# Performance work log

Measured on AMD Instinct MI355X. Metric: run time of the kernel, lower is better.

The kernel has to match this reference:

```python
import jax, jax.numpy as jnp
import numpy as np

M, N, IN_DIM, NITER = 32, 32, 1024, 100
ALPHA, SIGMA = 0.3, 16.0  # sigma default = max(m, n) / 2
BATCH = 16384


def setup_inputs() -> dict:
    key = jax.random.key(0)
    k1, k2 = jax.random.split(key)
    x = jax.random.normal(k1, (BATCH, IN_DIM), dtype=jnp.float32)
    weights = jax.random.normal(k2, (IN_DIM, M * N), dtype=jnp.float32)
    ii, jj = jnp.meshgrid(jnp.arange(M), jnp.arange(N), indexing='ij')
    locations = jnp.stack([ii.ravel(), jj.ravel()], axis=1).astype(jnp.int32)  # (m*n, 2), row-major like the generator
    return {"x": x, "weights": weights, "locations": locations, "current_iter": 10}


def reference(x, weights, locations, current_iter):
    # x: (B, in_dim); weights: (in_dim, m*n); locations: (m*n, 2)
    B = x.shape[0]
    # Euclidean distances from each sample to each neuron, via ||a-b||^2 expansion
    x2 = jnp.sum(x * x, axis=1, keepdims=True)            # (B, 1)
    w2 = jnp.sum(weights * weights, axis=0)[None, :]      # (1, m*n)
    d2 = jnp.clip(x2 + w2 - 2.0 * (x @ weights), 0.0, None)
    dists = jnp.sqrt(d2)                                  # (B, m*n)
    loss_per = jnp.min(dists, axis=1)                     # (B,)
    bmu_index = jnp.argmin(dists, axis=1)                 # (B,)
    iter_correction = 1.0 - current_iter / NITER
    lr = ALPHA * iter_correction
    sigma = SIGMA * iter_correction
    loc_f = locations.astype(jnp.float32)                 # (m*n, 2)
    bmu_loc = loc_f[bmu_index]                            # (B, 2)
    # squared grid distance of every neuron to each sample's BMU
    dsq = jnp.sum((loc_f[None, :, :] - bmu_loc[:, None, :]) ** 2, axis=2)  # (B, m*n)
    lr_locations = jnp.exp(-dsq / (sigma * sigma)) * lr   # (B, m*n)
    # delta[i,k] = (1/B) * sum_b lr_locations[b,k] * (x[b,i] - weights[i,k])
    # computed without materializing the (B, in_dim, m*n) broadcast tensor
    pos = jnp.einsum('bk,bi->ik', lr_locations, x)        # (in_dim, m*n)
    neg = weights * jnp.sum(lr_locations, axis=0)[None, :]
    delta = (pos - neg) / B
    new_weights = weights + delta
    loss = jnp.sum(loss_per) / B
    return loss, new_weights
```

## Files before the change

kernel.cpp:

```cpp
#include <hip/hip_runtime.h>

typedef unsigned short u16;
typedef short bf16x8 __attribute__((ext_vector_type(8)));
typedef float f32x4 __attribute__((ext_vector_type(4)));

#define BATCH   16384
#define INDIM   1024
#define KNEUR   1024

__device__ __forceinline__ u16 f2bf(float f) {
  union { float f; unsigned u; } v; v.f = f;
  unsigned r = v.u + 0x7FFFu + ((v.u >> 16) & 1u);
  return (u16)(r >> 16);
}
__device__ __forceinline__ float bf2f(u16 h) {
  union { unsigned u; float f; } v; v.u = ((unsigned)h) << 16; return v.f;
}

#define GLDS(gp, lp) __builtin_amdgcn_global_load_lds( \
  (const __attribute__((address_space(1))) void*)(gp), \
  (__attribute__((address_space(3))) void*)(lp), 16, 0, 0)

#define RAWBAR() __builtin_amdgcn_s_barrier()
#define LGKM0() do { asm volatile("s_waitcnt lgkmcnt(0)" ::: "memory"); \
                     __builtin_amdgcn_sched_barrier(0); } while (0)
#define VMC6() asm volatile("s_waitcnt vmcnt(6)" ::: "memory")
#define VMC0() asm volatile("s_waitcnt vmcnt(0)" ::: "memory")

__global__ __launch_bounds__(256)
void k_prep(const float* __restrict__ x, u16* __restrict__ xb, float* __restrict__ x2,
            const float* __restrict__ w, u16* __restrict__ wt, float* __restrict__ w2,
            const int* __restrict__ loc, const int* __restrict__ itp,
            u16* __restrict__ Tb, float* __restrict__ Tf,
            float* __restrict__ Xf, int* __restrict__ cntcur, float* __restrict__ S) {
  __shared__ float tile[64][65];
  __shared__ float red[4][64];
  int bid = blockIdx.x;
  int t = threadIdx.x;
  if (bid < 4096) {
    int row = bid * 4 + (t >> 6);
    int l = t & 63;
    const float* xr = x + (size_t)row * INDIM;
    u16* xbr = xb + (size_t)row * INDIM;
    float s = 0.f;
    #pragma unroll
    for (int seg = 0; seg < 4; ++seg) {
      float4 v = *(const float4*)(xr + seg * 256 + l * 4);
      ushort4 o; o.x = f2bf(v.x); o.y = f2bf(v.y); o.z = f2bf(v.z); o.w = f2bf(v.w);
      *(ushort4*)(xbr + seg * 256 + l * 4) = o;
      s += v.x * v.x + v.y * v.y + v.z * v.z + v.w * v.w;
    }
    for (int m = 32; m; m >>= 1) s += __shfl_xor(s, m, 64);
    if (l == 0) x2[row] = s;
  } else if (bid < 8192) {
    int id = (bid - 4096) * 256 + t;
    int c = id >> 10, k = id & 1023;
    float corr = 1.f - (float)itp[0] / 100.f;
    float lr = 0.3f * corr;
    float sig = 16.f * corr;
    float inv_s2 = 1.f / (sig * sig);
    int di = loc[2 * c] - loc[2 * k];
    int dj = loc[2 * c + 1] - loc[2 * k + 1];
    float v = lr * __expf(-(float)(di * di + dj * dj) * inv_s2);
    Tf[id] = v;
    Tb[id] = f2bf(v);
    Xf[id] = 0.f;
    if (id < 2048) cntcur[id] = 0;
    if (id < 1024) S[id] = 0.f;
  } else if (bid < 8448) {
    int bb = bid - 8192;
    int bi = bb & 15;
    int bj = bb >> 4;
    int tx = t & 63, ty = t >> 6;
    int i0 = bj * 64, k0 = bi * 64;
    for (int r = ty; r < 64; r += 4)
      tile[r][tx] = w[(size_t)(i0 + r) * KNEUR + k0 + tx];
    __syncthreads();
    for (int r = ty; r < 64; r += 4)
      wt[(size_t)(k0 + r) * INDIM + i0 + tx] = f2bf(tile[tx][r]);
  } else {
    int tx = t & 63, ty = t >> 6;
    int k = (bid - 8448) * 64 + tx;
    float s = 0.f;
    for (int i = ty * 256; i < ty * 256 + 256; ++i) {
      float v = w[(size_t)i * KNEUR + k];
      s += v * v;
    }
    red[ty][tx] = s;
    __syncthreads();
    if (ty == 0) w2[k] = red[0][tx] + red[1][tx] + red[2][tx] + red[3][tx];
  }
}

__global__ __launch_bounds__(512, 2)
void k_gemm1_8p(const u16* __restrict__ A, const u16* __restrict__ Bm,
                const float* __restrict__ x2, const float* __restrict__ w2,
                float* __restrict__ pmin, int* __restrict__ pidx) {
  __shared__ __align__(16) u16 lds[2][2][2][128 * 64];
  __shared__ float s_rv[2][256];
  __shared__ int   s_ri[2][256];

  int bid = blockIdx.x;
  int swz = (bid & 7) * 32 + (bid >> 3);
  int mb = swz >> 2, nb = swz & 3;
  int tid = threadIdx.x;
  int lane = tid & 63;
  int wm = (tid >> 6) >> 1, wn = (tid >> 6) & 1;

  const size_t rowA0 = (size_t)mb * 256;
  const size_t rowB0 = (size_t)nb * 256;

  auto STAGE = [&](int u, int op, int qh) {
    if (u >= 16) return;
    const u16* src = (op == 0) ? (A + (rowA0 + qh * 128) * 1024)
                               : (Bm + (rowB0 + qh * 128) * 1024);
    int k0 = u * 64;
    u16* dst0 = &lds[u & 1][op][qh][0];
    #pragma unroll
    for (int j = 0; j < 2; ++j) {
      int s = j * 512 + tid;
      int r = s >> 3;
      int cs = (s & 7) ^ (r & 7);
      GLDS(src + (size_t)r * 1024 + k0 + cs * 8, dst0 + (size_t)s * 8);
    }
  };
  auto LDA = [&](bf16x8 (&a)[2][2], int db, int qm) {
    #pragma unroll
    for (int mt = 0; mt < 2; ++mt)
      #pragma unroll
      for (int kk = 0; kk < 2; ++kk) {
        int row = wm * 32 + mt * 16 + (lane & 15);
        int ch = (kk * 4 + (lane >> 4)) ^ (row & 7);
        a[mt][kk] = *(const bf16x8*)(&lds[db][0][qm][row * 64 + ch * 8]);
      }
  };
  auto LDB = [&](bf16x8 (&b)[4][2], int db, int qn) {
    #pragma unroll
    for (int nt = 0; nt < 4; ++nt)
      #pragma unroll
      for (int kk = 0; kk < 2; ++kk) {
        int row = wn * 64 + nt * 16 + (lane & 15);
        int ch = (kk * 4 + (lane >> 4)) ^ (row & 7);
        b[nt][kk] = *(const bf16x8*)(&lds[db][1][qn][row * 64 + ch * 8]);
      }
  };

  f32x4 acc[2][2][2][4];
  #pragma unroll
  for (int i = 0; i < 2; ++i)
    #pragma unroll
    for (int j = 0; j < 2; ++j)
      #pragma unroll
      for (int m = 0; m < 2; ++m)
        #pragma unroll
        for (int n = 0; n < 4; ++n) {
          acc[i][j][m][n][0] = 0.f; acc[i][j][m][n][1] = 0.f;
          acc[i][j][m][n][2] = 0.f; acc[i][j][m][n][3] = 0.f;
        }

  bf16x8 a[2][2], b0[4][2], b1[4][2];

  #define PHASE(accq, av, bv) do { \
    __builtin_amdgcn_s_setprio(1); \
    _Pragma("unroll") \
    for (int mt = 0; mt < 2; ++mt) \
      _Pragma("unroll") \
      for (int nt = 0; nt < 4; ++nt) \
        _Pragma("unroll") \
        for (int kk = 0; kk < 2; ++kk) \
          accq[mt][nt] = __builtin_amdgcn_mfma_f32_16x16x32_bf16(av[mt][kk], bv[nt][kk], accq[mt][nt], 0, 0, 0); \
    __builtin_amdgcn_s_setprio(0); \
  } while (0)

  STAGE(0, 0, 0); STAGE(0, 1, 1); STAGE(0, 0, 1); STAGE(0, 1, 0);
  STAGE(1, 0, 0); STAGE(1, 1, 1); STAGE(1, 0, 1);
  VMC6();
  RAWBAR();

  for (int t = 0; t < 16; ++t) {
    int db = t & 1;
    LDA(a, db, 0); LDB(b0, db, 0);
    STAGE(t + 1, 1, 0);
    RAWBAR(); LGKM0();
    PHASE(acc[0][0], a, b0);
    RAWBAR();
    LDB(b1, db, 1);
    STAGE(t + 2, 0, 0);
    RAWBAR(); LGKM0();
    PHASE(acc[0][1], a, b1);
    RAWBAR();
    LDA(a, db, 1);
    STAGE(t + 2, 1, 1);
    RAWBAR(); LGKM0();
    PHASE(acc[1][1], a, b1);
    RAWBAR();
    STAGE(t + 2, 0, 1);
    RAWBAR(); LGKM0();
    PHASE(acc[1][0], a, b0);
    if (t < 14) { VMC6(); } else { VMC0(); }
    RAWBAR();
  }

  int g = lane >> 4, li = lane & 15;
  #pragma unroll
  for (int qm = 0; qm < 2; ++qm)
    #pragma unroll
    for (int mt = 0; mt < 2; ++mt)
      #pragma unroll
      for (int rr = 0; rr < 4; ++rr) {
        int lrow = qm * 128 + wm * 32 + mt * 16 + g * 4 + rr;
        float xv = x2[rowA0 + lrow];
        float v = 1e30f; int vi = 0x7fffffff;
        #pragma unroll
        for (int qn = 0; qn < 2; ++qn)
          #pragma unroll
          for (int nt = 0; nt < 4; ++nt) {
            int col = (int)rowB0 + qn * 128 + wn * 64 + nt * 16 + li;
            float d2 = xv + w2[col] - 2.f * acc[qm][qn][mt][nt][rr];
            if (d2 < v) { v = d2; vi = col; }
          }
        #pragma unroll
        for (int m = 1; m < 16; m <<= 1) {
          float ov = __shfl_xor(v, m, 64);
          int oi = __shfl_xor(vi, m, 64);
          if (ov < v || (ov == v && oi < vi)) { v = ov; vi = oi; }
        }
        if (li == 0) { s_rv[wn][lrow] = v; s_ri[wn][lrow] = vi; }
      }
  __syncthreads();
  if (tid < 256) {
    float v0 = s_rv[0][tid], v1 = s_rv[1][tid];
    int i0 = s_ri[0][tid], i1 = s_ri[1][tid];
    float v = v0; int vi = i0;
    if (v1 < v0 || (v1 == v0 && i1 < i0)) { v = v1; vi = i1; }
    size_t brow = rowA0 + tid;
    pmin[brow * 4 + nb] = v;
    pidx[brow * 4 + nb] = vi;
  }
  #undef PHASE
}

__global__ __launch_bounds__(256, 4)
void k_gemm2(const u16* __restrict__ A, const u16* __restrict__ Bm,
             float* __restrict__ P4) {
  __shared__ __align__(16) u16 ldsA[128 * 64];
  __shared__ __align__(16) u16 ldsB[128 * 64];

  int bid = blockIdx.x;
  int ks = bid & 3;
  int tile = bid >> 2;
  int mb = tile >> 3, nb = tile & 7;
  int ktlo = ks * 4, kthi = ktlo + 4;
  int lane = threadIdx.x & 63;
  int wid = threadIdx.x >> 6;
  int wr = wid >> 1, wc = wid & 1;

  f32x4 acc[4][4];
  #pragma unroll
  for (int i = 0; i < 4; ++i)
    #pragma unroll
    for (int j = 0; j < 4; ++j) { acc[i][j][0] = 0.f; acc[i][j][1] = 0.f; acc[i][j][2] = 0.f; acc[i][j][3] = 0.f; }

  const size_t rowA0 = (size_t)mb * 128;
  const size_t rowB0 = (size_t)nb * 128;

  for (int kt = ktlo; kt < kthi; ++kt) {
    int k0 = kt * 64;
    __syncthreads();
    #pragma unroll
    for (int q = 0; q < 4; ++q) {
      int p = q * 256 + wid * 64 + lane;
      int row = p >> 3;
      int clog = (p & 7) ^ (row & 7);
      GLDS(A + (rowA0 + row) * 1024 + k0 + clog * 8,
           ldsA + (size_t)(q * 256 + wid * 64) * 8);
    }
    #pragma unroll
    for (int q = 0; q < 4; ++q) {
      int p = q * 256 + wid * 64 + lane;
      int row = p >> 3;
      int clog = (p & 7) ^ (row & 7);
      GLDS(Bm + (rowB0 + row) * 1024 + k0 + clog * 8,
           ldsB + (size_t)(q * 256 + wid * 64) * 8);
    }
    __syncthreads();
    #pragma unroll
    for (int kk = 0; kk < 2; ++kk) {
      bf16x8 af[4], bfr[4];
      #pragma unroll
      for (int mt = 0; mt < 4; ++mt) {
        int row = wr * 64 + mt * 16 + (lane & 15);
        int ch = (kk * 4 + (lane >> 4)) ^ (row & 7);
        af[mt] = *(const bf16x8*)(ldsA + row * 64 + ch * 8);
      }
      #pragma unroll
      for (int nt = 0; nt < 4; ++nt) {
        int row = wc * 64 + nt * 16 + (lane & 15);
        int ch = (kk * 4 + (lane >> 4)) ^ (row & 7);
        bfr[nt] = *(const bf16x8*)(ldsB + row * 64 + ch * 8);
      }
      #pragma unroll
      for (int mt = 0; mt < 4; ++mt)
        #pragma unroll
        for (int nt = 0; nt < 4; ++nt)
          acc[mt][nt] = __builtin_amdgcn_mfma_f32_16x16x32_bf16(af[mt], bfr[nt], acc[mt][nt], 0, 0, 0);
    }
  }

  float* base = P4 + ((size_t)ks << 20);
  #pragma unroll
  for (int mt = 0; mt < 4; ++mt)
    #pragma unroll
    for (int nt = 0; nt < 4; ++nt)
      #pragma unroll
      for (int r = 0; r < 4; ++r) {
        int i = (int)rowA0 + wr * 64 + mt * 16 + (lane >> 4) * 4 + r;
        int k = (int)rowB0 + wc * 64 + nt * 16 + (lane & 15);
        base[(size_t)i * KNEUR + k] = acc[mt][nt][r];
      }
}

__global__ void k_bmu_count(const float* __restrict__ pmin, const int* __restrict__ pidx,
                            int* __restrict__ bmu, float* __restrict__ lpart,
                            int* __restrict__ cnt) {
  int b = blockIdx.x * 256 + threadIdx.x;
  float v = 1e30f; int vi = 0;
  #pragma unroll
  for (int j = 0; j < 4; ++j) {
    float pv = pmin[(size_t)b * 4 + j];
    if (pv < v) { v = pv; vi = pidx[(size_t)b * 4 + j]; }
  }
  bmu[b] = vi;
  atomicAdd(&cnt[vi], 1);
  float d = sqrtf(fmaxf(v, 0.f));
  __shared__ float red[256];
  red[threadIdx.x] = d;
  __syncthreads();
  for (int s = 128; s > 0; s >>= 1) {
    if (threadIdx.x < s) red[threadIdx.x] += red[threadIdx.x + s];
    __syncthreads();
  }
  if (threadIdx.x == 0) lpart[blockIdx.x] = red[0];
}

__global__ void k_offsets_loss(const int* __restrict__ cnt, int* __restrict__ cursor,
                               float* __restrict__ cntf,
                               const float* __restrict__ lpart, float* __restrict__ out) {
  __shared__ int sc[256];
  int t = threadIdx.x;
  int4 c4 = *(const int4*)(cnt + 4 * t);
  int tsum = c4.x + c4.y + c4.z + c4.w;
  sc[t] = tsum;
  __syncthreads();
  for (int off = 1; off < 256; off <<= 1) {
    int val = sc[t];
    int add = (t >= off) ? sc[t - off] : 0;
    __syncthreads();
    sc[t] = val + add;
    __syncthreads();
  }
  int excl = sc[t] - tsum;
  cursor[4 * t + 0] = excl;
  cursor[4 * t + 1] = excl + c4.x;
  cursor[4 * t + 2] = excl + c4.x + c4.y;
  cursor[4 * t + 3] = excl + c4.x + c4.y + c4.z;
  cntf[4 * t + 0] = (float)c4.x;
  cntf[4 * t + 1] = (float)c4.y;
  cntf[4 * t + 2] = (float)c4.z;
  cntf[4 * t + 3] = (float)c4.w;
  if (t < 64) {
    float l = lpart[t];
    for (int m = 32; m; m >>= 1) l += __shfl_xor(l, m, 64);
    if (t == 0) out[0] = l * (1.f / (float)BATCH);
  }
}

__global__ void k_place_S(const int* __restrict__ bmu, int* __restrict__ cursor,
                          int* __restrict__ perm,
                          const float* __restrict__ cntf, const float* __restrict__ Tf,
                          float* __restrict__ S) {
  int bid = blockIdx.x;
  int t = threadIdx.x;
  if (bid < 64) {
    int b = bid * 256 + t;
    int c = bmu[b];
    int p = atomicAdd(&cursor[c], 1);
    perm[p] = b;
  } else {
    int chunk = bid - 64;
    int cchunk = chunk >> 2;
    int kb = chunk & 3;
    int k = kb * 256 + t;
    float s = 0.f;
    for (int c = cchunk * 64; c < cchunk * 64 + 64; ++c)
      s += cntf[c] * Tf[(size_t)c * KNEUR + k];
    atomicAdd(&S[k], s);
  }
}

__global__ __launch_bounds__(256)
void k_xsum2(const int* __restrict__ perm, const int* __restrict__ bmu,
             const u16* __restrict__ xb, float* __restrict__ Xf) {
  int t = threadIdx.x;
  int m0 = blockIdx.x * 16;
  int pm[16], cl[16];
  #pragma unroll
  for (int j = 0; j < 16; ++j) pm[j] = perm[m0 + j];
  #pragma unroll
  for (int j = 0; j < 16; ++j) cl[j] = bmu[pm[j]];
  float a0 = 0.f, a1 = 0.f, a2 = 0.f, a3 = 0.f;
  int ccur = cl[0];
  #pragma unroll
  for (int j = 0; j < 16; ++j) {
    if (cl[j] != ccur) {
      float* p = Xf + (size_t)ccur * INDIM + 4 * t;
      atomicAdd(p + 0, a0); atomicAdd(p + 1, a1);
      atomicAdd(p + 2, a2); atomicAdd(p + 3, a3);
      a0 = a1 = a2 = a3 = 0.f;
      ccur = cl[j];
    }
    ushort4 v = *(const ushort4*)(xb + (size_t)pm[j] * INDIM + t * 4);
    a0 += bf2f(v.x); a1 += bf2f(v.y); a2 += bf2f(v.z); a3 += bf2f(v.w);
  }
  float* p = Xf + (size_t)ccur * INDIM + 4 * t;
  atomicAdd(p + 0, a0); atomicAdd(p + 1, a1);
  atomicAdd(p + 2, a2); atomicAdd(p + 3, a3);
}

__global__ void k_trans_base(const float* __restrict__ Xf, u16* __restrict__ xst,
                             const float* __restrict__ w, const float* __restrict__ S,
                             float* __restrict__ outw) {
  int bid = blockIdx.x;
  int t = threadIdx.x;
  if (bid < 256) {
    __shared__ float tile[64][65];
    int bc = bid & 15;
    int bi = bid >> 4;
    int tx = t & 63, ty = t >> 6;
    int c0 = bc * 64, i0 = bi * 64;
    for (int r = ty; r < 64; r += 4)
      tile[r][tx] = Xf[(size_t)(c0 + r) * INDIM + i0 + tx];
    __syncthreads();
    for (int r = ty; r < 64; r += 4)
      xst[(size_t)(i0 + r) * KNEUR + c0 + tx] = f2bf(tile[tx][r]);
  } else {
    const float invB = 1.f / (float)BATCH;
    size_t base = ((size_t)(bid - 256) * 256 + t) * 16;
    int k = (int)(base & 1023);
    #pragma unroll
    for (int seg = 0; seg < 4; ++seg) {
      float4 wv = *(const float4*)(w + base + seg * 4);
      float4 sv = *(const float4*)(S + k + seg * 4);
      outw[base + seg * 4 + 0] = wv.x - wv.x * sv.x * invB;
      outw[base + seg * 4 + 1] = wv.y - wv.y * sv.y * invB;
      outw[base + seg * 4 + 2] = wv.z - wv.z * sv.z * invB;
      outw[base + seg * 4 + 3] = wv.w - wv.w * sv.w * invB;
    }
  }
}

__global__ void k_wupd(const float* __restrict__ P4, float* __restrict__ outw) {
  const float invB = 1.f / (float)BATCH;
  int id4 = blockIdx.x * 256 + threadIdx.x;
  size_t base = (size_t)id4 * 4;
  float4 p0 = *(const float4*)(P4 + base);
  float4 p1 = *(const float4*)(P4 + (1u << 20) + base);
  float4 p2 = *(const float4*)(P4 + (2u << 20) + base);
  float4 p3 = *(const float4*)(P4 + (3u << 20) + base);
  outw[base + 0] += (p0.x + p1.x + p2.x + p3.x) * invB;
  outw[base + 1] += (p0.y + p1.y + p2.y + p3.y) * invB;
  outw[base + 2] += (p0.z + p1.z + p2.z + p3.z) * invB;
  outw[base + 3] += (p0.w + p1.w + p2.w + p3.w) * invB;
}

extern "C" void kernel_launch(void* const* d_in, const int* in_sizes, int n_in,
                              void* d_out, int out_size, void* d_ws, size_t ws_size,
                              hipStream_t stream) {
  const float* x = (const float*)d_in[0];
  const float* w = (const float*)d_in[1];
  const int* loc = (const int*)d_in[2];
  const int* it = (const int*)d_in[3];
  float* out = (float*)d_out;

  char* ws = (char*)d_ws;
  size_t off = 0;
  auto alloc = [&](size_t bytes) -> void* {
    void* p = ws + off;
    off += (bytes + 255) & ~(size_t)255;
    return p;
  };
  u16* xb    = (u16*)  alloc((size_t)BATCH * INDIM * 2);
  u16* wt    = (u16*)  alloc((size_t)KNEUR * INDIM * 2);
  u16* Tb    = (u16*)  alloc((size_t)KNEUR * KNEUR * 2);
  float* Tf  = (float*)alloc((size_t)KNEUR * KNEUR * 4);
  u16* xst   = (u16*)  alloc((size_t)INDIM * KNEUR * 2);
  float* x2  = (float*)alloc((size_t)BATCH * 4);
  float* w2  = (float*)alloc((size_t)KNEUR * 4);
  float* pmin= (float*)alloc((size_t)BATCH * 4 * 4);
  int* pidx  = (int*)  alloc((size_t)BATCH * 4 * 4);
  int* bmu   = (int*)  alloc((size_t)BATCH * 4);
  float* cntf= (float*)alloc((size_t)KNEUR * 4);
  float* S   = (float*)alloc((size_t)KNEUR * 4);
  float* lpart=(float*)alloc(64 * 4);
  float* Xf  = (float*)alloc((size_t)KNEUR * INDIM * 4);
  int* cntcur= (int*)  alloc((size_t)2 * KNEUR * 4);
  int* perm  = (int*)  alloc((size_t)BATCH * 4);
  if (off > ws_size) return;

  int* cnt = cntcur;
  int* cursor = cntcur + KNEUR;
  float* outw = out + 1;
  float* P4 = (float*)xb;

  k_prep<<<8464, 256, 0, stream>>>(x, xb, x2, w, wt, w2, loc, it, Tb, Tf, Xf, cntcur, S);
  k_gemm1_8p<<<256, 512, 0, stream>>>(xb, wt, x2, w2, pmin, pidx);
  k_bmu_count<<<64, 256, 0, stream>>>(pmin, pidx, bmu, lpart, cnt);
  k_offsets_loss<<<1, 256, 0, stream>>>(cnt, cursor, cntf, lpart, out);
  k_place_S<<<128, 256, 0, stream>>>(bmu, cursor, perm, cntf, Tf, S);
  k_xsum2<<<BATCH / 16, 256, 0, stream>>>(perm, bmu, xb, Xf);
  k_trans_base<<<512, 256, 0, stream>>>(Xf, xst, w, S, outw);
  k_gemm2<<<256, 256, 0, stream>>>(xst, Tb, P4);
  k_wupd<<<1024, 256, 0, stream>>>(P4, outw);
}
```

Before: 142.7 us.

## Fuse BMU count and offset scan via last-block ticket, widen xsum chunks

Merges the BMU counting kernel and the single-block prefix-scan/loss kernel into one launch, where the last block to finish (found with an atomic ticket) performs the scan. This removes one kernel launch and its gap. It also doubles the samples per block in the Xf accumulation kernel to cut the number of atomics, and adds a partial lgkmcnt wait in the GEMM1 main loop. The ticket counter gets zeroed in prep, and the fusion relies on a threadfence so the last block sees the other blocks' counts.

```diff
diff --git a/kernel.cpp b/kernel.cpp
--- a/kernel.cpp
+++ b/kernel.cpp
@@ -24,6 +24,7 @@
 #define RAWBAR() __builtin_amdgcn_s_barrier()
 #define LGKM0() do { asm volatile("s_waitcnt lgkmcnt(0)" ::: "memory"); \
                      __builtin_amdgcn_sched_barrier(0); } while (0)
+#define LGKM8() asm volatile("s_waitcnt lgkmcnt(8)" ::: "memory")
 #define VMC6() asm volatile("s_waitcnt vmcnt(6)" ::: "memory")
 #define VMC0() asm volatile("s_waitcnt vmcnt(0)" ::: "memory")
 
@@ -65,7 +66,7 @@
     Tf[id] = v;
     Tb[id] = f2bf(v);
     Xf[id] = 0.f;
-    if (id < 2048) cntcur[id] = 0;
+    if (id < 2304) cntcur[id] = 0;
     if (id < 1024) S[id] = 0.f;
   } else if (bid < 8448) {
     int bb = bid - 8192;
@@ -181,6 +182,7 @@
     int db = t & 1;
     LDA(a, db, 0); LDB(b0, db, 0);
     STAGE(t + 1, 1, 0);
+    LGKM8();
     RAWBAR(); LGKM0();
     PHASE(acc[0][0], a, b0);
     RAWBAR();
@@ -320,10 +322,13 @@
       }
 }
 
-__global__ void k_bmu_count(const float* __restrict__ pmin, const int* __restrict__ pidx,
-                            int* __restrict__ bmu, float* __restrict__ lpart,
-                            int* __restrict__ cnt) {
-  int b = blockIdx.x * 256 + threadIdx.x;
+__global__ void k_bmu_scan(const float* __restrict__ pmin, const int* __restrict__ pidx,
+                           int* __restrict__ bmu, float* __restrict__ lpart,
+                           int* __restrict__ cnt, int* __restrict__ ticket,
+                           int* __restrict__ cursor, float* __restrict__ cntf,
+                           float* __restrict__ out) {
+  int t = threadIdx.x;
+  int b = blockIdx.x * 256 + t;
   float v = 1e30f; int vi = 0;
   #pragma unroll
   for (int j = 0; j < 4; ++j) {
@@ -334,20 +339,21 @@
   atomicAdd(&cnt[vi], 1);
   float d = sqrtf(fmaxf(v, 0.f));
   __shared__ float red[256];
-  red[threadIdx.x] = d;
+  red[t] = d;
   __syncthreads();
   for (int s = 128; s > 0; s >>= 1) {
-    if (threadIdx.x < s) red[threadIdx.x] += red[threadIdx.x + s];
-    __syncthreads();
-  }
-  if (threadIdx.x == 0) lpart[blockIdx.x] = red[0];
-}
-
-__global__ void k_offsets_loss(const int* __restrict__ cnt, int* __restrict__ cursor,
-                               float* __restrict__ cntf,
-                               const float* __restrict__ lpart, float* __restrict__ out) {
+    if (t < s) red[t] += red[t + s];
+    __syncthreads();
+  }
+  if (t == 0) lpart[blockIdx.x] = red[0];
+
+  __threadfence();
+  __shared__ int is_last;
+  if (t == 0) is_last = (atomicAdd(ticket, 1) == 63);
+  __syncthreads();
+  if (!is_last) return;
+
   __shared__ int sc[256];
-  int t = threadIdx.x;
   int4 c4 = *(const int4*)(cnt + 4 * t);
   int tsum = c4.x + c4.y + c4.z + c4.w;
   sc[t] = tsum;
@@ -402,16 +408,16 @@
 void k_xsum2(const int* __restrict__ perm, const int* __restrict__ bmu,
              const u16* __restrict__ xb, float* __restrict__ Xf) {
   int t = threadIdx.x;
-  int m0 = blockIdx.x * 16;
-  int pm[16], cl[16];
-  #pragma unroll
-  for (int j = 0; j < 16; ++j) pm[j] = perm[m0 + j];
-  #pragma unroll
-  for (int j = 0; j < 16; ++j) cl[j] = bmu[pm[j]];
+  int m0 = blockIdx.x * 32;
+  int pm[32], cl[32];
+  #pragma unroll
+  for (int j = 0; j < 32; ++j) pm[j] = perm[m0 + j];
+  #pragma unroll
+  for (int j = 0; j < 32; ++j) cl[j] = bmu[pm[j]];
   float a0 = 0.f, a1 = 0.f, a2 = 0.f, a3 = 0.f;
   int ccur = cl[0];
   #pragma unroll
-  for (int j = 0; j < 16; ++j) {
+  for (int j = 0; j < 32; ++j) {
     if (cl[j] != ccur) {
       float* p = Xf + (size_t)ccur * INDIM + 4 * t;
       atomicAdd(p + 0, a0); atomicAdd(p + 1, a1);
@@ -503,21 +509,21 @@
   float* S   = (float*)alloc((size_t)KNEUR * 4);
   float* lpart=(float*)alloc(64 * 4);
   float* Xf  = (float*)alloc((size_t)KNEUR * INDIM * 4);
-  int* cntcur= (int*)  alloc((size_t)2 * KNEUR * 4);
+  int* cntcur= (int*)  alloc((size_t)2304 * 4);
   int* perm  = (int*)  alloc((size_t)BATCH * 4);
   if (off > ws_size) return;
 
   int* cnt = cntcur;
   int* cursor = cntcur + KNEUR;
+  int* ticket = cntcur + 2 * KNEUR;
   float* outw = out + 1;
   float* P4 = (float*)xb;
 
   k_prep<<<8464, 256, 0, stream>>>(x, xb, x2, w, wt, w2, loc, it, Tb, Tf, Xf, cntcur, S);
   k_gemm1_8p<<<256, 512, 0, stream>>>(xb, wt, x2, w2, pmin, pidx);
-  k_bmu_count<<<64, 256, 0, stream>>>(pmin, pidx, bmu, lpart, cnt);
-  k_offsets_loss<<<1, 256, 0, stream>>>(cnt, cursor, cntf, lpart, out);
+  k_bmu_scan<<<64, 256, 0, stream>>>(pmin, pidx, bmu, lpart, cnt, ticket, cursor, cntf, out);
   k_place_S<<<128, 256, 0, stream>>>(bmu, cursor, perm, cntf, Tf, S);
-  k_xsum2<<<BATCH / 16, 256, 0, stream>>>(perm, bmu, xb, Xf);
+  k_xsum2<<<BATCH / 32, 256, 0, stream>>>(perm, bmu, xb, Xf);
   k_trans_base<<<512, 256, 0, stream>>>(Xf, xst, w, S, outw);
   k_gemm2<<<256, 256, 0, stream>>>(xst, Tb, P4);
   k_wupd<<<1024, 256, 0, stream>>>(P4, outw);
```

Result: faster. 139.7 us (-2.1%).
